# Optimization experiments

Measured on AMD Instinct MI355X. Metric: run time of the kernel, lower is better.

Reference implementation:

```python
import jax, jax.numpy as jnp
import numpy as np

CAPACITY = 0.5  # top_k = int(seq_len * capacity)

def setup_inputs() -> dict:
    key = jax.random.key(0)
    k1, k2, k3, k4 = jax.random.split(key, 4)
    b, s, d, d_ff = 4, 4096, 1024, 4096
    x = jax.random.normal(k1, (b, s, d), dtype=jnp.float32)
    mask = jnp.ones((b, s), dtype=jnp.bool_)
    # learned params: router (Linear(d,1,bias=False)) and the block MLP
    Wr = jax.random.normal(k2, (d, 1), dtype=jnp.float32) * (d ** -0.5)
    W1 = jax.random.normal(k3, (d, d_ff), dtype=jnp.float32) * (d ** -0.5)
    W2 = jax.random.normal(k4, (d_ff, d), dtype=jnp.float32) * (d_ff ** -0.5)
    return {"x": x, "mask": mask, "Wr": Wr, "W1": W1, "W2": W2}

def reference(x, mask, Wr, W1, W2):
    b, s, d = x.shape
    top_k = int(s * CAPACITY)
    # router logits [b, s]
    logits = (x @ Wr)[..., 0]
    # top-k over sequence dim (torch sorted=False; softmax/gather are
    # permutation-equivariant so sorted top_k gives identical results)
    vals, idx = jax.lax.top_k(logits, top_k)          # [b, k]
    order = jnp.argsort(idx, axis=1)                  # sort selected indices ascending
    sel = jnp.take_along_axis(idx, order, axis=1)     # [b, k] token positions, ascending
    w = jax.nn.softmax(vals, axis=1)                  # softmax over selected logits
    r_w = jnp.take_along_axis(w, order, axis=1)       # weights reordered to match sel
    # gather selected tokens
    fx = jnp.take_along_axis(x, sel[..., None], axis=1)  # [b, k, d]
    # block: residual MLP whose update is scaled by router weights (mask unused by MLP)
    h = jax.nn.silu(fx @ W1) @ W2
    out = fx + h * r_w[..., None]
    # scatter processed tokens back into x
    batch = jnp.arange(b)[:, None]
    hidden_states = x.at[batch, sel].set(out)
    # aux loss: faithful to the original (flat view + flat index set, then BCE-with-logits mean)
    flat_logits = logits.reshape(-1)                  # [b*s]
    targets = jnp.zeros_like(flat_logits).at[sel.reshape(-1)].set(1.0)
    aux_loss = jnp.mean(
        jnp.maximum(flat_logits, 0.0)
        - flat_logits * targets
        + jnp.log1p(jnp.exp(-jnp.abs(flat_logits)))
    )
    return hidden_states, aux_loss
```

## Files before the change

kernel.cpp:

```cpp
#include <hip/hip_runtime.h>
#include <hip/hip_bf16.h>
#include <cstdint>

#define B_ 4
#define S_ 4096
#define D_ 1024
#define DFF_ 4096
#define KSEL_ 2048
#define M_ (B_ * KSEL_)
#define NTOK_ (B_ * S_)

typedef short bf16x8 __attribute__((ext_vector_type(8)));
typedef float f32x4 __attribute__((ext_vector_type(4)));

__device__ inline unsigned short f2bf(float f) {
    union { float f; unsigned int u; } c; c.f = f;
    unsigned int u = c.u;
    unsigned int r = u + 0x7fffu + ((u >> 16) & 1u);
    return (unsigned short)(r >> 16);
}

__global__ __launch_bounds__(256)
void transpose_bf16(const float* __restrict__ src, unsigned short* __restrict__ dst,
                    int R, int C) {
    __shared__ float tile[32][33];
    int c0 = blockIdx.x * 32, r0 = blockIdx.y * 32;
    for (int i = threadIdx.y; i < 32; i += 8)
        tile[i][threadIdx.x] = src[(size_t)(r0 + i) * C + c0 + threadIdx.x];
    __syncthreads();
    for (int i = threadIdx.y; i < 32; i += 8)
        dst[(size_t)(c0 + i) * R + r0 + threadIdx.x] = f2bf(tile[threadIdx.x][i]);
}

__global__ __launch_bounds__(256)
void router_kernel(const float* __restrict__ x, const float* __restrict__ Wr,
                   float* __restrict__ logits, unsigned short* __restrict__ xb,
                   float* __restrict__ out) {
    int wid = threadIdx.x >> 6, lane = threadIdx.x & 63;
    int row = blockIdx.x * 4 + wid;
    const float* xr = x + (size_t)row * D_;
    unsigned short* xbr = xb + (size_t)row * D_;
    float* outr = out + (size_t)row * D_;
    float acc = 0.f;
#pragma unroll
    for (int j = 0; j < 4; j++) {
        int off = j * 256 + lane * 4;
        float4 v = *(const float4*)(xr + off);
        float4 w = *(const float4*)(Wr + off);
        acc += v.x * w.x + v.y * w.y + v.z * w.z + v.w * w.w;
        *(float4*)(outr + off) = v;
        ushort4 o;
        o.x = f2bf(v.x); o.y = f2bf(v.y); o.z = f2bf(v.z); o.w = f2bf(v.w);
        *(ushort4*)(xbr + off) = o;
    }
#pragma unroll
    for (int s = 32; s; s >>= 1) acc += __shfl_xor(acc, s);
    if (lane == 0) logits[row] = acc;
}

__global__ __launch_bounds__(256)
void rank_partial_kernel(const float* __restrict__ logits, int* __restrict__ rank) {
    __shared__ float lj[512];
    int b  = blockIdx.x >> 7;
    int ic = (blockIdx.x >> 3) & 15;
    int jc = blockIdx.x & 7;
    const float* L = logits + b * S_;
    for (int t = threadIdx.x; t < 512; t += 256) lj[t] = L[jc * 512 + t];
    __syncthreads();
    int i = ic * 256 + threadIdx.x;
    float li = L[i];
    int jbase = jc * 512;
    int r = 0;
    const float4* __restrict__ lj4 = (const float4*)lj;
#pragma unroll 4
    for (int q = 0; q < 128; q++) {
        float4 v = lj4[q];
        int jb = jbase + q * 4;
        r += (v.x > li) | ((v.x == li) & (jb     < i));
        r += (v.y > li) | ((v.y == li) & (jb + 1 < i));
        r += (v.z > li) | ((v.z == li) & (jb + 2 < i));
        r += (v.w > li) | ((v.w == li) & (jb + 3 < i));
    }
    atomicAdd(&rank[b * S_ + i], r);
}

__global__ __launch_bounds__(256)
void compact_kernel(const float* __restrict__ logits, const int* __restrict__ rank,
                    int* __restrict__ flags,
                    int* __restrict__ rowidx, float* __restrict__ rw) {
    __shared__ float lg[S_];
    __shared__ int f[S_];
    __shared__ int tsum[256];
    __shared__ float red[256];
    int b = blockIdx.x;
    const float* L = logits + b * S_;
    const int* R = rank + b * S_;
    int* F = flags + b * S_;
    for (int j = threadIdx.x; j < S_ / 4; j += 256) {
        ((float4*)lg)[j] = ((const float4*)L)[j];
        int4 rk = ((const int4*)R)[j];
        int4 fl;
        fl.x = rk.x < KSEL_; fl.y = rk.y < KSEL_;
        fl.z = rk.z < KSEL_; fl.w = rk.w < KSEL_;
        ((int4*)f)[j] = fl;
        ((int4*)F)[j] = fl;
    }
    __syncthreads();
    float mx = -INFINITY;
    for (int j = threadIdx.x; j < S_; j += 256) mx = fmaxf(mx, lg[j]);
    red[threadIdx.x] = mx; __syncthreads();
    for (int s = 128; s; s >>= 1) {
        if (threadIdx.x < s) red[threadIdx.x] = fmaxf(red[threadIdx.x], red[threadIdx.x + s]);
        __syncthreads();
    }
    float m = red[0];
    __syncthreads();

    float esum = 0.f;
    int s0 = 0;
#pragma unroll
    for (int j = 0; j < 16; j++) {
        int i = threadIdx.x * 16 + j;
        s0 += f[i];
        if (f[i]) esum += expf(lg[i] - m);
    }
    red[threadIdx.x] = esum; __syncthreads();
    for (int s = 128; s; s >>= 1) {
        if (threadIdx.x < s) red[threadIdx.x] += red[threadIdx.x + s];
        __syncthreads();
    }
    float inv = 1.f / red[0];

    tsum[threadIdx.x] = s0; __syncthreads();
    for (int s = 1; s < 256; s <<= 1) {
        int u = (threadIdx.x >= s) ? tsum[threadIdx.x - s] : 0;
        __syncthreads();
        tsum[threadIdx.x] += u;
        __syncthreads();
    }
    int pos = tsum[threadIdx.x] - s0;
    for (int j = 0; j < 16; j++) {
        int i = threadIdx.x * 16 + j;
        if (f[i]) {
            rowidx[b * KSEL_ + pos] = b * S_ + i;
            rw[b * KSEL_ + pos] = expf(lg[i] - m) * inv;
            pos++;
        }
    }
}

__global__ __launch_bounds__(256)
void loss_kernel(const float* __restrict__ logits, const int* __restrict__ flags,
                 float* __restrict__ partials) {
    __shared__ float red[256];
    int i = blockIdx.x * 256 + threadIdx.x;
    float l = logits[i];
    float t = 0.f;
    if (i < S_)
        t = (flags[i] | flags[S_ + i] | flags[2 * S_ + i] | flags[3 * S_ + i]) ? 1.f : 0.f;
    float v = fmaxf(l, 0.f) - l * t + log1pf(expf(-fabsf(l)));
    red[threadIdx.x] = v; __syncthreads();
    for (int s = 128; s; s >>= 1) {
        if (threadIdx.x < s) red[threadIdx.x] += red[threadIdx.x + s];
        __syncthreads();
    }
    if (threadIdx.x == 0) partials[blockIdx.x] = red[0];
}

__global__ void loss_final(const float* __restrict__ partials, float* __restrict__ out) {
    float v = partials[threadIdx.x];
#pragma unroll
    for (int s = 32; s; s >>= 1) v += __shfl_xor(v, s);
    if (threadIdx.x == 0) out[0] = v / (float)NTOK_;
}

template <int MODE, int N, int K>
__global__ __launch_bounds__(512, 2)
void gemm_pipe_kernel(const unsigned short* __restrict__ A,
                      const unsigned short* __restrict__ BT,
                      const int* __restrict__ rowidx,
                      const float* __restrict__ rw,
                      const float* __restrict__ x,
                      unsigned short* __restrict__ Hout,
                      float* __restrict__ Out) {
    constexpr int BM = 128, BN = 256, BK = 64;
    constexpr int KI = K / BK;
    constexpr int NT = N / BN;
    constexpr int MT = M_ / BM;
    constexpr int NWG = NT * MT;
    constexpr int CPX = NWG / 8;
    __shared__ __attribute__((aligned(16))) unsigned short As[3][BM * BK];
    __shared__ __attribute__((aligned(16))) unsigned short Bs[3][BN * BK];

    const int tid = threadIdx.x;
    const int w = tid >> 6, lane = tid & 63;
    const int wm = w >> 2, wn = w & 3;

    int wgid = blockIdx.y * NT + blockIdx.x;
    int swz = (wgid & 7) * CPX + (wgid >> 3);
    const int tile_n = (swz % NT) * BN;
    const int tile_m = (swz / NT) * BM;

    const int srow = lane >> 3;
    const int sw = (lane & 7) ^ srow;
    const uint64_t abase = (uint64_t)(uintptr_t)A;
    const uint64_t bbase = (uint64_t)(uintptr_t)BT;
    uint64_t aaddr[2], baddr[4];
#pragma unroll
    for (int t = 0; t < 2; ++t) {
        int r = t * 64 + w * 8 + srow;
        int ar = (MODE == 1) ? rowidx[tile_m + r] : (tile_m + r);
        aaddr[t] = abase + ((uint64_t)ar * K + (uint64_t)sw * 8) * 2ull;
    }
#pragma unroll
    for (int t = 0; t < 4; ++t) {
        int r = t * 64 + w * 8 + srow;
        baddr[t] = bbase + ((uint64_t)(tile_n + r) * K + (uint64_t)sw * 8) * 2ull;
    }

    auto stage = [&](int kt, int slot) {
        const uint64_t koff = (uint64_t)kt * (BK * 2);
#pragma unroll
        for (int t = 0; t < 2; ++t) {
            unsigned short* lds = &As[slot][(t * 64 + w * 8) * BK];
            __builtin_amdgcn_global_load_lds(
                (const __attribute__((address_space(1))) unsigned int*)(uintptr_t)(aaddr[t] + koff),
                (__attribute__((address_space(3))) unsigned int*)lds, 16, 0, 0);
        }
#pragma unroll
        for (int t = 0; t < 4; ++t) {
            unsigned short* lds = &Bs[slot][(t * 64 + w * 8) * BK];
            __builtin_amdgcn_global_load_lds(
                (const __attribute__((address_space(1))) unsigned int*)(uintptr_t)(baddr[t] + koff),
                (__attribute__((address_space(3))) unsigned int*)lds, 16, 0, 0);
        }
    };

    f32x4 acc[4][4];
#pragma unroll
    for (int i = 0; i < 4; i++)
#pragma unroll
        for (int j = 0; j < 4; j++) acc[i][j] = (f32x4){0.f, 0.f, 0.f, 0.f};

    stage(0, 0);
    stage(1, 1);
    asm volatile("s_waitcnt vmcnt(6)" ::: "memory");
    __builtin_amdgcn_s_barrier();

    const int lr = lane & 15, quad = lane >> 4;
    int s_cur = 0;
    for (int kt = 0; kt < KI; ++kt) {
        int s_pre = s_cur + 2; if (s_pre >= 3) s_pre -= 3;
        if (kt + 2 < KI) stage(kt + 2, s_pre);

        bf16x8 af[4][2], bfr[4][2];
#pragma unroll
        for (int m4 = 0; m4 < 4; ++m4) {
            int row = wm * 64 + m4 * 16 + lr;
#pragma unroll
            for (int ks = 0; ks < 2; ++ks) {
                int kc = ks * 4 + quad;
                af[m4][ks] = *(const bf16x8*)((const char*)&As[s_cur][0]
                                + row * (BK * 2) + ((kc ^ (lr & 7)) * 16));
            }
        }
#pragma unroll
        for (int n4 = 0; n4 < 4; ++n4) {
            int col = wn * 64 + n4 * 16 + lr;
#pragma unroll
            for (int ks = 0; ks < 2; ++ks) {
                int kc = ks * 4 + quad;
                bfr[n4][ks] = *(const bf16x8*)((const char*)&Bs[s_cur][0]
                                + col * (BK * 2) + ((kc ^ (lr & 7)) * 16));
            }
        }

        __builtin_amdgcn_s_setprio(1);
#pragma unroll
        for (int ks = 0; ks < 2; ++ks)
#pragma unroll
            for (int m4 = 0; m4 < 4; ++m4)
#pragma unroll
                for (int n4 = 0; n4 < 4; ++n4)
                    acc[m4][n4] = __builtin_amdgcn_mfma_f32_16x16x32_bf16(
                        af[m4][ks], bfr[n4][ks], acc[m4][n4], 0, 0, 0);
        __builtin_amdgcn_s_setprio(0);

        if (kt + 2 < KI) {
            asm volatile("s_waitcnt vmcnt(6)" ::: "memory");
        } else {
            asm volatile("s_waitcnt vmcnt(0)" ::: "memory");
        }
        __builtin_amdgcn_s_barrier();
        s_cur += 1; if (s_cur >= 3) s_cur = 0;
    }

    if (MODE == 1) {
#pragma unroll
        for (int m4 = 0; m4 < 4; ++m4)
#pragma unroll
            for (int r = 0; r < 4; ++r) {
                int m = tile_m + wm * 64 + m4 * 16 + quad * 4 + r;
#pragma unroll
                for (int n4 = 0; n4 < 4; ++n4) {
                    int col = tile_n + wn * 64 + n4 * 16 + lr;
                    float v = acc[m4][n4][r];
                    v = v / (1.f + __expf(-v));
                    Hout[(uint64_t)m * N + col] = f2bf(v);
                }
            }
    } else {
#pragma unroll
        for (int m4 = 0; m4 < 4; ++m4)
#pragma unroll
            for (int r = 0; r < 4; ++r) {
                int m = tile_m + wm * 64 + m4 * 16 + quad * 4 + r;
                int grow = rowidx[m];
                float wgt = rw[m];
                uint64_t rb = (uint64_t)grow * D_;
#pragma unroll
                for (int n4 = 0; n4 < 4; ++n4) {
                    int col = tile_n + wn * 64 + n4 * 16 + lr;
                    Out[rb + col] = x[rb + col] + acc[m4][n4][r] * wgt;
                }
            }
    }
}

extern "C" void kernel_launch(void* const* d_in, const int* in_sizes, int n_in,
                              void* d_out, int out_size, void* d_ws, size_t ws_size,
                              hipStream_t stream) {
    const float* x  = (const float*)d_in[0];
    const float* Wr = (const float*)d_in[2];
    const float* W1 = (const float*)d_in[3];
    const float* W2 = (const float*)d_in[4];
    float* out = (float*)d_out;

    char* ws = (char*)d_ws;
    size_t off = 0;
    auto alloc = [&](size_t bytes) {
        char* p = ws + off;
        off = (off + bytes + 255) & ~(size_t)255;
        return p;
    };
    unsigned short* xb   = (unsigned short*)alloc((size_t)NTOK_ * D_ * 2);
    unsigned short* W1bT = (unsigned short*)alloc((size_t)DFF_ * D_ * 2);
    unsigned short* W2bT = (unsigned short*)alloc((size_t)D_ * DFF_ * 2);
    unsigned short* H    = (unsigned short*)alloc((size_t)M_ * DFF_ * 2);
    float* logits  = (float*)alloc(NTOK_ * 4);
    int*   rank    = (int*)alloc(NTOK_ * 4);
    int*   flags   = (int*)alloc(NTOK_ * 4);
    int*   rowidx  = (int*)alloc(M_ * 4);
    float* rwp     = (float*)alloc(M_ * 4);
    float* partials = (float*)alloc(64 * 4);

    (void)hipMemsetAsync(rank, 0, NTOK_ * 4, stream);

    transpose_bf16<<<dim3(DFF_ / 32, D_ / 32), dim3(32, 8), 0, stream>>>(W1, W1bT, D_, DFF_);
    transpose_bf16<<<dim3(D_ / 32, DFF_ / 32), dim3(32, 8), 0, stream>>>(W2, W2bT, DFF_, D_);
    router_kernel<<<NTOK_ / 4, 256, 0, stream>>>(x, Wr, logits, xb, out);
    rank_partial_kernel<<<512, 256, 0, stream>>>(logits, rank);
    compact_kernel<<<B_, 256, 0, stream>>>(logits, rank, flags, rowidx, rwp);
    loss_kernel<<<NTOK_ / 256, 256, 0, stream>>>(logits, flags, partials);
    loss_final<<<1, 64, 0, stream>>>(partials, out + (size_t)NTOK_ * D_);
    gemm_pipe_kernel<1, DFF_, D_><<<dim3(DFF_ / 256, M_ / 128), 512, 0, stream>>>(
        xb, W1bT, rowidx, nullptr, nullptr, H, nullptr);
    gemm_pipe_kernel<2, D_, DFF_><<<dim3(D_ / 256, M_ / 128), 512, 0, stream>>>(
        H, W2bT, rowidx, rwp, x, nullptr, out);
}
```

Before: 395.9 us.

## Split GEMM k-step into two phases interleaving LDS reads, prefetch and MFMA

Restructures the GEMM main loop so that each BK tile is processed in two k-halves. Each half reads its LDS fragments, issues part of the next-stage global-to-LDS prefetch, and then runs its MFMA batch between explicit barriers. The goal is to spread memory traffic across the MFMA work and hold fewer fragment registers live at once, in the style of a ping-pong schedule. The cost is extra barriers per iteration, and the hand-placed waitcnt logic carries correctness risk.

```diff
diff --git a/kernel.cpp b/kernel.cpp
--- a/kernel.cpp
+++ b/kernel.cpp
@@ -218,22 +218,20 @@
         baddr[t] = bbase + ((uint64_t)(tile_n + r) * K + (uint64_t)sw * 8) * 2ull;
     }
 
-    auto stage = [&](int kt, int slot) {
+    auto gload = [&](unsigned short* lds, uint64_t gaddr) {
+        __builtin_amdgcn_global_load_lds(
+            (const __attribute__((address_space(1))) unsigned int*)(uintptr_t)gaddr,
+            (__attribute__((address_space(3))) unsigned int*)lds, 16, 0, 0);
+    };
+
+    auto stage_full = [&](int kt, int slot) {
         const uint64_t koff = (uint64_t)kt * (BK * 2);
 #pragma unroll
-        for (int t = 0; t < 2; ++t) {
-            unsigned short* lds = &As[slot][(t * 64 + w * 8) * BK];
-            __builtin_amdgcn_global_load_lds(
-                (const __attribute__((address_space(1))) unsigned int*)(uintptr_t)(aaddr[t] + koff),
-                (__attribute__((address_space(3))) unsigned int*)lds, 16, 0, 0);
-        }
-#pragma unroll
-        for (int t = 0; t < 4; ++t) {
-            unsigned short* lds = &Bs[slot][(t * 64 + w * 8) * BK];
-            __builtin_amdgcn_global_load_lds(
-                (const __attribute__((address_space(1))) unsigned int*)(uintptr_t)(baddr[t] + koff),
-                (__attribute__((address_space(3))) unsigned int*)lds, 16, 0, 0);
-        }
+        for (int t = 0; t < 2; ++t)
+            gload(&As[slot][(t * 64 + w * 8) * BK], aaddr[t] + koff);
+#pragma unroll
+        for (int t = 0; t < 4; ++t)
+            gload(&Bs[slot][(t * 64 + w * 8) * BK], baddr[t] + koff);
     };
 
     f32x4 acc[4][4];
@@ -242,57 +240,91 @@
 #pragma unroll
         for (int j = 0; j < 4; j++) acc[i][j] = (f32x4){0.f, 0.f, 0.f, 0.f};
 
-    stage(0, 0);
-    stage(1, 1);
+    stage_full(0, 0);
+    stage_full(1, 1);
     asm volatile("s_waitcnt vmcnt(6)" ::: "memory");
-    __builtin_amdgcn_s_barrier();
+    asm volatile("s_barrier" ::: "memory");
 
     const int lr = lane & 15, quad = lane >> 4;
-    int s_cur = 0;
+    int c = 0;
     for (int kt = 0; kt < KI; ++kt) {
-        int s_pre = s_cur + 2; if (s_pre >= 3) s_pre -= 3;
-        if (kt + 2 < KI) stage(kt + 2, s_pre);
-
-        bf16x8 af[4][2], bfr[4][2];
-#pragma unroll
-        for (int m4 = 0; m4 < 4; ++m4) {
-            int row = wm * 64 + m4 * 16 + lr;
-#pragma unroll
-            for (int ks = 0; ks < 2; ++ks) {
-                int kc = ks * 4 + quad;
-                af[m4][ks] = *(const bf16x8*)((const char*)&As[s_cur][0]
-                                + row * (BK * 2) + ((kc ^ (lr & 7)) * 16));
-            }
-        }
-#pragma unroll
-        for (int n4 = 0; n4 < 4; ++n4) {
-            int col = wn * 64 + n4 * 16 + lr;
-#pragma unroll
-            for (int ks = 0; ks < 2; ++ks) {
-                int kc = ks * 4 + quad;
-                bfr[n4][ks] = *(const bf16x8*)((const char*)&Bs[s_cur][0]
-                                + col * (BK * 2) + ((kc ^ (lr & 7)) * 16));
-            }
-        }
-
-        __builtin_amdgcn_s_setprio(1);
-#pragma unroll
-        for (int ks = 0; ks < 2; ++ks)
+        int pre = c + 2; if (pre >= 3) pre -= 3;
+        const char* Abase_l = (const char*)&As[c][0];
+        const char* Bbase_l = (const char*)&Bs[c][0];
+        const bool do_stage = (kt + 2 < KI);
+        const uint64_t koff = (uint64_t)(kt + 2) * (BK * 2);
+
+        {
+            bf16x8 af[4], bfr[4];
+            const int xo = (quad ^ (lr & 7)) * 16;
+#pragma unroll
+            for (int m4 = 0; m4 < 4; ++m4) {
+                int row = wm * 64 + m4 * 16 + lr;
+                af[m4] = *(const bf16x8*)(Abase_l + row * (BK * 2) + xo);
+            }
+#pragma unroll
+            for (int n4 = 0; n4 < 4; ++n4) {
+                int col = wn * 64 + n4 * 16 + lr;
+                bfr[n4] = *(const bf16x8*)(Bbase_l + col * (BK * 2) + xo);
+            }
+            if (do_stage) {
+#pragma unroll
+                for (int t = 0; t < 2; ++t)
+                    gload(&As[pre][(t * 64 + w * 8) * BK], aaddr[t] + koff);
+                gload(&Bs[pre][(w * 8) * BK], baddr[0] + koff);
+            }
+            asm volatile("s_barrier" ::: "memory");
+            asm volatile("s_waitcnt lgkmcnt(0)" ::: "memory");
+            __builtin_amdgcn_sched_barrier(0);
+            __builtin_amdgcn_s_setprio(1);
 #pragma unroll
             for (int m4 = 0; m4 < 4; ++m4)
 #pragma unroll
                 for (int n4 = 0; n4 < 4; ++n4)
                     acc[m4][n4] = __builtin_amdgcn_mfma_f32_16x16x32_bf16(
-                        af[m4][ks], bfr[n4][ks], acc[m4][n4], 0, 0, 0);
-        __builtin_amdgcn_s_setprio(0);
-
-        if (kt + 2 < KI) {
-            asm volatile("s_waitcnt vmcnt(6)" ::: "memory");
-        } else {
-            asm volatile("s_waitcnt vmcnt(0)" ::: "memory");
+                        af[m4], bfr[n4], acc[m4][n4], 0, 0, 0);
+            __builtin_amdgcn_s_setprio(0);
+            asm volatile("s_barrier" ::: "memory");
         }
-        __builtin_amdgcn_s_barrier();
-        s_cur += 1; if (s_cur >= 3) s_cur = 0;
+
+        {
+            bf16x8 af[4], bfr[4];
+            const int xo = ((4 + quad) ^ (lr & 7)) * 16;
+#pragma unroll
+            for (int m4 = 0; m4 < 4; ++m4) {
+                int row = wm * 64 + m4 * 16 + lr;
+                af[m4] = *(const bf16x8*)(Abase_l + row * (BK * 2) + xo);
+            }
+#pragma unroll
+            for (int n4 = 0; n4 < 4; ++n4) {
+                int col = wn * 64 + n4 * 16 + lr;
+                bfr[n4] = *(const bf16x8*)(Bbase_l + col * (BK * 2) + xo);
+            }
+            if (do_stage) {
+#pragma unroll
+                for (int t = 1; t < 4; ++t)
+                    gload(&Bs[pre][(t * 64 + w * 8) * BK], baddr[t] + koff);
+            }
+            asm volatile("s_barrier" ::: "memory");
+            asm volatile("s_waitcnt lgkmcnt(0)" ::: "memory");
+            __builtin_amdgcn_sched_barrier(0);
+            __builtin_amdgcn_s_setprio(1);
+#pragma unroll
+            for (int m4 = 0; m4 < 4; ++m4)
+#pragma unroll
+                for (int n4 = 0; n4 < 4; ++n4)
+                    acc[m4][n4] = __builtin_amdgcn_mfma_f32_16x16x32_bf16(
+                        af[m4], bfr[n4], acc[m4][n4], 0, 0, 0);
+            __builtin_amdgcn_s_setprio(0);
+            if (kt + 2 < KI) {
+                asm volatile("s_waitcnt vmcnt(6)" ::: "memory");
+            } else if (kt + 1 < KI) {
+                asm volatile("s_waitcnt vmcnt(0)" ::: "memory");
+            }
+            asm volatile("s_barrier" ::: "memory");
+        }
+
+        c += 1; if (c >= 3) c = 0;
     }
 
     if (MODE == 1) {
```

Result: faster. 361.9 us (-8.6%).
